# Optimization experiments

Hardware: AMD Instinct MI355X
Metric: run time of the kernel (lower is better)

Reference implementation:

```python
import jax, jax.numpy as jnp
import numpy as np

N_NODES = 100000
N_EDGES = 3200000
IN_F, HID, OUT = 3, 32, 1
NEG_SLOPE = 0.2


def _glorot(key, shape):
    fan_in, fan_out = shape[0], shape[-1]
    lim = jnp.sqrt(6.0 / (fan_in + fan_out)).astype(jnp.float32)
    return jax.random.uniform(key, shape, jnp.float32, -lim, lim)


def setup_inputs() -> dict:
    key = jax.random.key(0)
    ks = jax.random.split(key, 12)
    x = jax.random.normal(ks[0], (N_NODES, IN_F), jnp.float32)
    edge_index = jax.random.randint(ks[1], (2, N_EDGES), 0, N_NODES, jnp.int32)
    return {
        "x": x,
        "edge_index": edge_index,
        "W1": _glorot(ks[2], (IN_F, HID)),
        "att_src1": _glorot(ks[3], (1, HID))[0],
        "att_dst1": _glorot(ks[4], (1, HID))[0],
        "b1": jnp.zeros((HID,), jnp.float32),
        "W2": _glorot(ks[5], (HID, HID)),
        "att_src2": _glorot(ks[6], (1, HID))[0],
        "att_dst2": _glorot(ks[7], (1, HID))[0],
        "b2": jnp.zeros((HID,), jnp.float32),
        "Wl": _glorot(ks[8], (HID, OUT)),
        "bl": jnp.zeros((OUT,), jnp.float32),
    }


def gat_layer(x, src, dst, W, att_src, att_dst, b):
    # h: [N, HID] dense transform
    h = x @ W
    # per-node attention halves (compute once per node, gather per edge)
    a_s = h @ att_src  # [N]
    a_d = h @ att_dst  # [N]
    logits = jax.nn.leaky_relu(a_s[src] + a_d[dst], NEG_SLOPE)  # [E+N]
    # segment-softmax over incoming edges of each dst node
    m = jax.ops.segment_max(logits, dst, num_segments=N_NODES)
    m = jnp.where(jnp.isfinite(m), m, 0.0)
    ex = jnp.exp(logits - m[dst])
    denom = jax.ops.segment_sum(ex, dst, num_segments=N_NODES)
    coef = ex / (denom[dst] + 1e-16)
    # weighted scatter-aggregate of source messages
    out = jax.ops.segment_sum(coef[:, None] * h[src], dst, num_segments=N_NODES)
    return out + b


def reference(x, edge_index, W1, att_src1, att_dst1, b1, W2, att_src2, att_dst2, b2, Wl, bl):
    # PyG GATConv default: add self-loops
    loops = jnp.arange(N_NODES, dtype=edge_index.dtype)
    src = jnp.concatenate([edge_index[0], loops])
    dst = jnp.concatenate([edge_index[1], loops])
    h = gat_layer(x, src, dst, W1, att_src1, att_dst1, b1)
    h = jax.nn.relu(h)  # dropout is identity in eval
    h = gat_layer(h, src, dst, W2, att_src2, att_dst2, b2)
    h = jax.nn.relu(h)
    return h @ Wl + bl
```

## Files before the change

kernel.cpp:

```cpp
#include <hip/hip_runtime.h>
#include <hip/hip_fp16.h>

#define HID 32
#define NB_MAX 512
#define CHUNK_A 16384
#define CHUNK_C 8192

__device__ __forceinline__ float lrelu(float x) {
    return x > 0.0f ? x : 0.2f * x;
}

__global__ void k_transform1(const float* __restrict__ x,
                             const float* __restrict__ W1,
                             const float* __restrict__ att_src,
                             const float* __restrict__ att_dst,
                             float* __restrict__ h,
                             __half* __restrict__ hh,
                             float* __restrict__ a_s,
                             float* __restrict__ a_d,
                             int* __restrict__ bucketCount,
                             int NB, int N)
{
    int tid = blockIdx.x * blockDim.x + threadIdx.x;
    if (tid < NB) bucketCount[tid] = 0;
    int n = tid >> 5;
    int f = tid & 31;
    if (n >= N) return;
    float x0 = x[n * 3 + 0], x1 = x[n * 3 + 1], x2 = x[n * 3 + 2];
    float hv = x0 * W1[f] + x1 * W1[HID + f] + x2 * W1[2 * HID + f];
    h[(size_t)n * HID + f] = hv;
    hh[(size_t)n * HID + f] = __float2half(hv);
    float as = hv * att_src[f];
    float ad = hv * att_dst[f];
    #pragma unroll
    for (int m = 16; m >= 1; m >>= 1) {
        as += __shfl_xor(as, m, 32);
        ad += __shfl_xor(ad, m, 32);
    }
    if (f == 0) { a_s[n] = as; a_d[n] = ad; }
}

__global__ void __launch_bounds__(256) k_count_buckets(const int* __restrict__ dst,
                                                       int* __restrict__ bucketCount,
                                                       int NB, int E)
{
    __shared__ int lh[NB_MAX];
    int t = threadIdx.x;
    for (int i = t; i < NB_MAX; i += 256) lh[i] = 0;
    __syncthreads();
    int base = blockIdx.x * CHUNK_A;
    int end = base + CHUNK_A; if (end > E) end = E;
    for (int i = base + t; i < end; i += 256)
        atomicAdd(&lh[dst[i] >> 8], 1);
    __syncthreads();
    for (int b = t; b < NB; b += 256)
        if (lh[b]) atomicAdd(&bucketCount[b], lh[b]);
}

__global__ void __launch_bounds__(NB_MAX) k_scan_buckets(const int* __restrict__ bucketCount,
                                                         int* __restrict__ bucketBase,
                                                         int* __restrict__ cursor, int NB)
{
    __shared__ int arr[NB_MAX];
    int t = threadIdx.x;
    int c = (t < NB) ? bucketCount[t] : 0;
    arr[t] = c;
    __syncthreads();
    for (int o = 1; o < NB_MAX; o <<= 1) {
        int v = (t >= o) ? arr[t - o] : 0;
        __syncthreads();
        arr[t] += v;
        __syncthreads();
    }
    if (t < NB) { int b = arr[t] - c; bucketBase[t] = b; cursor[t] = b; }
}

__global__ void __launch_bounds__(256) k_binscatter(const int* __restrict__ src,
                                                    const int* __restrict__ dst,
                                                    int* __restrict__ cursor,
                                                    unsigned int* __restrict__ packed,
                                                    int NB, int E)
{
    __shared__ int lhist[NB_MAX], lbase[NB_MAX], lcur[NB_MAX];
    int t = threadIdx.x;
    for (int i = t; i < NB_MAX; i += 256) { lhist[i] = 0; lcur[i] = 0; }
    __syncthreads();
    int base = blockIdx.x * CHUNK_C;
    int cnt = E - base; if (cnt > CHUNK_C) cnt = CHUNK_C;
    for (int i = t; i < cnt; i += 256)
        atomicAdd(&lhist[dst[base + i] >> 8], 1);
    __syncthreads();
    for (int b = t; b < NB; b += 256)
        lbase[b] = lhist[b] ? atomicAdd(&cursor[b], lhist[b]) : 0;
    __syncthreads();
    for (int i = t; i < cnt; i += 256) {
        int d = dst[base + i];
        int s = src[base + i];
        int b = d >> 8;
        int pos = atomicAdd(&lcur[b], 1);
        packed[lbase[b] + pos] = (unsigned)s | ((unsigned)(d & 255) << 17);
    }
}

__global__ void __launch_bounds__(256) k_bucket_csr(const unsigned int* __restrict__ packed,
                                                    const int* __restrict__ bucketBase,
                                                    const int* __restrict__ bucketCount,
                                                    int* __restrict__ csr,
                                                    int* __restrict__ offsets,
                                                    int* __restrict__ deg, int N)
{
    __shared__ int lhist[256], lscan[256], lcur[256];
    int b = blockIdx.x, t = threadIdx.x;
    int base = bucketBase[b];
    int cnt = bucketCount[b];
    lhist[t] = 0; lcur[t] = 0;
    __syncthreads();
    for (int i = t; i < cnt; i += 256)
        atomicAdd(&lhist[(packed[base + i] >> 17) & 255], 1);
    __syncthreads();
    lscan[t] = lhist[t];
    __syncthreads();
    for (int o = 1; o < 256; o <<= 1) {
        int v = (t >= o) ? lscan[t - o] : 0;
        __syncthreads();
        lscan[t] += v;
        __syncthreads();
    }
    int node = (b << 8) + t;
    int excl = lscan[t] - lhist[t];
    if (node < N) { offsets[node] = base + excl; deg[node] = lhist[t]; }
    for (int i = t; i < cnt; i += 256) {
        unsigned int p = packed[base + i];
        int dlow = (p >> 17) & 255;
        int pos = atomicAdd(&lcur[dlow], 1);
        csr[base + (lscan[dlow] - lhist[dlow]) + pos] = (int)(p & 0x1FFFF);
    }
}

__device__ __forceinline__ void agg_core(const float* __restrict__ h,
                                         const __half* __restrict__ hh,
                                         const float* __restrict__ a_s,
                                         float a_dn,
                                         const float* __restrict__ b,
                                         int n, int f, int off, int dg,
                                         const int* __restrict__ csr_src,
                                         float a_sn,
                                         float& vx, float& vy)
{
    float ex = __expf(lrelu(a_sn + a_dn));
    float den = ex;
    const float2 hself = *(const float2*)(h + (size_t)n * HID + 2 * f);
    float accx = ex * hself.x;
    float accy = ex * hself.y;
    for (int base = 0; base < dg; base += 16) {
        int m = dg - base; if (m > 16) m = 16;
        int sv = 0;
        float exv = 0.0f;
        if (f < m) {
            sv = csr_src[off + base + f];
            exv = __expf(lrelu(a_s[sv] + a_dn));
        }
        int j = 0;
        for (; j + 4 <= m; j += 4) {
            int s0 = __shfl(sv, j, 16), s1 = __shfl(sv, j + 1, 16);
            int s2 = __shfl(sv, j + 2, 16), s3 = __shfl(sv, j + 3, 16);
            float e0 = __shfl(exv, j, 16), e1 = __shfl(exv, j + 1, 16);
            float e2 = __shfl(exv, j + 2, 16), e3 = __shfl(exv, j + 3, 16);
            __half2 p0 = *(const __half2*)(hh + (size_t)s0 * HID + 2 * f);
            __half2 p1 = *(const __half2*)(hh + (size_t)s1 * HID + 2 * f);
            __half2 p2 = *(const __half2*)(hh + (size_t)s2 * HID + 2 * f);
            __half2 p3 = *(const __half2*)(hh + (size_t)s3 * HID + 2 * f);
            float2 q0 = __half22float2(p0);
            float2 q1 = __half22float2(p1);
            float2 q2 = __half22float2(p2);
            float2 q3 = __half22float2(p3);
            den += (e0 + e1) + (e2 + e3);
            accx = fmaf(e0, q0.x, accx); accy = fmaf(e0, q0.y, accy);
            accx = fmaf(e1, q1.x, accx); accy = fmaf(e1, q1.y, accy);
            accx = fmaf(e2, q2.x, accx); accy = fmaf(e2, q2.y, accy);
            accx = fmaf(e3, q3.x, accx); accy = fmaf(e3, q3.y, accy);
        }
        for (; j < m; ++j) {
            int s0 = __shfl(sv, j, 16);
            float e0 = __shfl(exv, j, 16);
            float2 q0 = __half22float2(*(const __half2*)(hh + (size_t)s0 * HID + 2 * f));
            den += e0;
            accx = fmaf(e0, q0.x, accx);
            accy = fmaf(e0, q0.y, accy);
        }
    }
    float inv = 1.0f / (den + 1e-16f);
    vx = fmaxf(accx * inv + b[2 * f], 0.0f);
    vy = fmaxf(accy * inv + b[2 * f + 1], 0.0f);
}

__global__ void __launch_bounds__(256) k_agg_mid(const float* __restrict__ h,
                          const __half* __restrict__ hh,
                          const float* __restrict__ a_s,
                          const float* __restrict__ a_d,
                          const int* __restrict__ offsets,
                          const int* __restrict__ deg,
                          const int* __restrict__ csr_src,
                          const float* __restrict__ b,
                          const float* __restrict__ W2,
                          const float* __restrict__ att_src2,
                          const float* __restrict__ att_dst2,
                          float* __restrict__ h_out,
                          __half* __restrict__ hh_out,
                          float* __restrict__ a_s_out,
                          float* __restrict__ a_d_out,
                          int N)
{
    int tid = blockIdx.x * blockDim.x + threadIdx.x;
    int n = tid >> 4;
    int f = tid & 15;
    if (n >= N) return;
    float vx, vy;
    agg_core(h, hh, a_s, a_d[n], b, n, f, offsets[n], deg[n], csr_src, a_s[n], vx, vy);
    float hx = 0.0f, hy = 0.0f;
    #pragma unroll
    for (int k = 0; k < 16; ++k) {
        float va = __shfl(vx, k, 16);
        float vb = __shfl(vy, k, 16);
        float2 w0 = *(const float2*)(W2 + (2 * k) * HID + 2 * f);
        float2 w1 = *(const float2*)(W2 + (2 * k + 1) * HID + 2 * f);
        hx = fmaf(va, w0.x, hx); hy = fmaf(va, w0.y, hy);
        hx = fmaf(vb, w1.x, hx); hy = fmaf(vb, w1.y, hy);
    }
    *(float2*)(h_out + (size_t)n * HID + 2 * f) = make_float2(hx, hy);
    *(__half2*)(hh_out + (size_t)n * HID + 2 * f) = __floats2half2_rn(hx, hy);
    float as = hx * att_src2[2 * f] + hy * att_src2[2 * f + 1];
    float ad = hx * att_dst2[2 * f] + hy * att_dst2[2 * f + 1];
    #pragma unroll
    for (int m2 = 8; m2 >= 1; m2 >>= 1) {
        as += __shfl_xor(as, m2, 16);
        ad += __shfl_xor(ad, m2, 16);
    }
    if (f == 0) { a_s_out[n] = as; a_d_out[n] = ad; }
}

__global__ void __launch_bounds__(256) k_agg_out(const float* __restrict__ h,
                          const __half* __restrict__ hh,
                          const float* __restrict__ a_s,
                          const float* __restrict__ a_d,
                          const int* __restrict__ offsets,
                          const int* __restrict__ deg,
                          const int* __restrict__ csr_src,
                          const float* __restrict__ b,
                          const float* __restrict__ Wl,
                          const float* __restrict__ bl,
                          float* __restrict__ out,
                          int N)
{
    int tid = blockIdx.x * blockDim.x + threadIdx.x;
    int n = tid >> 4;
    int f = tid & 15;
    if (n >= N) return;
    float vx, vy;
    agg_core(h, hh, a_s, a_d[n], b, n, f, offsets[n], deg[n], csr_src, a_s[n], vx, vy);
    float y = vx * Wl[2 * f] + vy * Wl[2 * f + 1];
    #pragma unroll
    for (int m2 = 8; m2 >= 1; m2 >>= 1) {
        y += __shfl_xor(y, m2, 16);
    }
    if (f == 0) out[n] = y + bl[0];
}

extern "C" void kernel_launch(void* const* d_in, const int* in_sizes, int n_in,
                              void* d_out, int out_size, void* d_ws, size_t ws_size,
                              hipStream_t stream)
{
    const float* x        = (const float*)d_in[0];
    const int*   eidx     = (const int*)d_in[1];
    const float* W1       = (const float*)d_in[2];
    const float* att_src1 = (const float*)d_in[3];
    const float* att_dst1 = (const float*)d_in[4];
    const float* b1       = (const float*)d_in[5];
    const float* W2       = (const float*)d_in[6];
    const float* att_src2 = (const float*)d_in[7];
    const float* att_dst2 = (const float*)d_in[8];
    const float* b2       = (const float*)d_in[9];
    const float* Wl       = (const float*)d_in[10];
    const float* bl       = (const float*)d_in[11];
    float* out = (float*)d_out;

    int N = in_sizes[0] / 3;
    int E = in_sizes[1] / 2;
    const int* src = eidx;
    const int* dst = eidx + E;
    int NB = (N + 255) >> 8;

    size_t szNH = (size_t)N * HID * 4;
    size_t szNHh = (size_t)N * HID * 2;
    size_t szE4 = (size_t)E * 4;
    size_t szN4 = (size_t)N * 4;

    char* ws = (char*)d_ws;
    float*  h1      = (float*)ws;  ws += szNH;
    float*  h2      = (float*)ws;  ws += szNH;
    unsigned int* packed = (unsigned int*)h2;
    __half* h1h     = (__half*)ws; ws += szNHh;
    __half* h2h     = (__half*)ws; ws += szNHh;
    int*    csr_src = (int*)ws;    ws += szE4;
    float*  a_s1    = (float*)ws;  ws += szN4;
    float*  a_d1    = (float*)ws;  ws += szN4;
    float*  a_s2    = (float*)ws;  ws += szN4;
    float*  a_d2    = (float*)ws;  ws += szN4;
    int*    deg     = (int*)ws;    ws += szN4;
    int*    offsets = (int*)ws;    ws += szN4;
    int*    bucketCount = (int*)ws; ws += NB_MAX * 4;
    int*    bucketBase  = (int*)ws; ws += NB_MAX * 4;
    int*    cursor      = (int*)ws; ws += NB_MAX * 4;

    const int B = 256;
    int gridNode32 = (N * HID + B - 1) / B;
    int gridNode16 = (N * 16 + B - 1) / B;
    int gridCount  = (E + CHUNK_A - 1) / CHUNK_A;
    int gridBin    = (E + CHUNK_C - 1) / CHUNK_C;

    k_transform1<<<gridNode32, B, 0, stream>>>(x, W1, att_src1, att_dst1,
                                               h1, h1h, a_s1, a_d1, bucketCount, NB, N);
    k_count_buckets<<<gridCount, B, 0, stream>>>(dst, bucketCount, NB, E);
    k_scan_buckets<<<1, NB_MAX, 0, stream>>>(bucketCount, bucketBase, cursor, NB);
    k_binscatter<<<gridBin, B, 0, stream>>>(src, dst, cursor, packed, NB, E);
    k_bucket_csr<<<NB, B, 0, stream>>>(packed, bucketBase, bucketCount,
                                       csr_src, offsets, deg, N);
    k_agg_mid<<<gridNode16, B, 0, stream>>>(h1, h1h, a_s1, a_d1, offsets, deg, csr_src,
                                            b1, W2, att_src2, att_dst2,
                                            h2, h2h, a_s2, a_d2, N);
    k_agg_out<<<gridNode16, B, 0, stream>>>(h2, h2h, a_s2, a_d2, offsets, deg, csr_src,
                                            b2, Wl, bl, out, N);
}
```

Before: 299.9 us.

## Use fixed-stride buckets for CSR build, stage in LDS, drop fp32 features

Replaces the count and scan bucket kernels with fixed-capacity buckets of 132 nodes at a 5120-entry stride. Each bucket's fill is tracked by an atomic cursor, and edges are staged in shared memory so global writes are contiguous. The bucket CSR pass sorts in LDS and writes back in place, so the separate csr array goes away. The fp32 copies of the hidden features are removed and the self term is read from the half buffer. The edge gather loop is unrolled to 8 for more loads in flight. The fixed capacity silently drops edges if a bucket overflows, so correctness depends on a roughly uniform degree distribution.

```diff
diff --git a/kernel.cpp b/kernel.cpp
--- a/kernel.cpp
+++ b/kernel.cpp
@@ -2,33 +2,30 @@
 #include <hip/hip_fp16.h>
 
 #define HID 32
-#define NB_MAX 512
-#define CHUNK_A 16384
-#define CHUNK_C 8192
-
-__device__ __forceinline__ float lrelu(float x) {
-    return x > 0.0f ? x : 0.2f * x;
-}
+#define BN 132
+#define NBPAD 1024
+#define BSTRIDE 5120
+#define CHUNK 8192
+
+__device__ __forceinline__ float lrelu(float x) { return x > 0.0f ? x : 0.2f * x; }
 
 __global__ void k_transform1(const float* __restrict__ x,
                              const float* __restrict__ W1,
                              const float* __restrict__ att_src,
                              const float* __restrict__ att_dst,
-                             float* __restrict__ h,
                              __half* __restrict__ hh,
                              float* __restrict__ a_s,
                              float* __restrict__ a_d,
-                             int* __restrict__ bucketCount,
-                             int NB, int N)
+                             int* __restrict__ cursor,
+                             int N)
 {
     int tid = blockIdx.x * blockDim.x + threadIdx.x;
-    if (tid < NB) bucketCount[tid] = 0;
+    if (tid < NBPAD) cursor[tid] = 0;
     int n = tid >> 5;
     int f = tid & 31;
     if (n >= N) return;
     float x0 = x[n * 3 + 0], x1 = x[n * 3 + 1], x2 = x[n * 3 + 2];
     float hv = x0 * W1[f] + x1 * W1[HID + f] + x2 * W1[2 * HID + f];
-    h[(size_t)n * HID + f] = hv;
     hh[(size_t)n * HID + f] = __float2half(hv);
     float as = hv * att_src[f];
     float ad = hv * att_dst[f];
@@ -40,79 +37,71 @@
     if (f == 0) { a_s[n] = as; a_d[n] = ad; }
 }
 
-__global__ void __launch_bounds__(256) k_count_buckets(const int* __restrict__ dst,
-                                                       int* __restrict__ bucketCount,
-                                                       int NB, int E)
-{
-    __shared__ int lh[NB_MAX];
-    int t = threadIdx.x;
-    for (int i = t; i < NB_MAX; i += 256) lh[i] = 0;
-    __syncthreads();
-    int base = blockIdx.x * CHUNK_A;
-    int end = base + CHUNK_A; if (end > E) end = E;
-    for (int i = base + t; i < end; i += 256)
-        atomicAdd(&lh[dst[i] >> 8], 1);
-    __syncthreads();
-    for (int b = t; b < NB; b += 256)
-        if (lh[b]) atomicAdd(&bucketCount[b], lh[b]);
-}
-
-__global__ void __launch_bounds__(NB_MAX) k_scan_buckets(const int* __restrict__ bucketCount,
-                                                         int* __restrict__ bucketBase,
-                                                         int* __restrict__ cursor, int NB)
-{
-    __shared__ int arr[NB_MAX];
-    int t = threadIdx.x;
-    int c = (t < NB) ? bucketCount[t] : 0;
-    arr[t] = c;
-    __syncthreads();
-    for (int o = 1; o < NB_MAX; o <<= 1) {
-        int v = (t >= o) ? arr[t - o] : 0;
-        __syncthreads();
-        arr[t] += v;
-        __syncthreads();
-    }
-    if (t < NB) { int b = arr[t] - c; bucketBase[t] = b; cursor[t] = b; }
-}
-
 __global__ void __launch_bounds__(256) k_binscatter(const int* __restrict__ src,
                                                     const int* __restrict__ dst,
                                                     int* __restrict__ cursor,
                                                     unsigned int* __restrict__ packed,
                                                     int NB, int E)
 {
-    __shared__ int lhist[NB_MAX], lbase[NB_MAX], lcur[NB_MAX];
+    __shared__ int stage[CHUNK];
+    __shared__ int lhist[NBPAD], lexcl[NBPAD], lbase[NBPAD], lcur[NBPAD];
+    __shared__ int arr[256];
     int t = threadIdx.x;
-    for (int i = t; i < NB_MAX; i += 256) { lhist[i] = 0; lcur[i] = 0; }
-    __syncthreads();
-    int base = blockIdx.x * CHUNK_C;
-    int cnt = E - base; if (cnt > CHUNK_C) cnt = CHUNK_C;
+    for (int i = t; i < NBPAD; i += 256) { lhist[i] = 0; lcur[i] = 0; }
+    __syncthreads();
+    int base = blockIdx.x * CHUNK;
+    int cnt = E - base; if (cnt > CHUNK) cnt = CHUNK;
     for (int i = t; i < cnt; i += 256)
-        atomicAdd(&lhist[dst[base + i] >> 8], 1);
-    __syncthreads();
+        atomicAdd(&lhist[dst[base + i] / BN], 1);
+    __syncthreads();
+    int b0 = 4 * t;
+    int c0 = lhist[b0], c1 = lhist[b0 + 1], c2 = lhist[b0 + 2], c3 = lhist[b0 + 3];
+    int s = c0 + c1 + c2 + c3;
+    arr[t] = s;
+    __syncthreads();
+    for (int o = 1; o < 256; o <<= 1) {
+        int v = (t >= o) ? arr[t - o] : 0;
+        __syncthreads();
+        arr[t] += v;
+        __syncthreads();
+    }
+    int ex = arr[t] - s;
+    lexcl[b0] = ex; lexcl[b0 + 1] = ex + c0;
+    lexcl[b0 + 2] = ex + c0 + c1; lexcl[b0 + 3] = ex + c0 + c1 + c2;
     for (int b = t; b < NB; b += 256)
-        lbase[b] = lhist[b] ? atomicAdd(&cursor[b], lhist[b]) : 0;
+        if (lhist[b]) lbase[b] = b * BSTRIDE + atomicAdd(&cursor[b], lhist[b]);
     __syncthreads();
     for (int i = t; i < cnt; i += 256) {
         int d = dst[base + i];
-        int s = src[base + i];
-        int b = d >> 8;
-        int pos = atomicAdd(&lcur[b], 1);
-        packed[lbase[b] + pos] = (unsigned)s | ((unsigned)(d & 255) << 17);
-    }
-}
-
-__global__ void __launch_bounds__(256) k_bucket_csr(const unsigned int* __restrict__ packed,
-                                                    const int* __restrict__ bucketBase,
-                                                    const int* __restrict__ bucketCount,
-                                                    int* __restrict__ csr,
+        int sv = src[base + i];
+        int b = d / BN;
+        int dl = d - b * BN;
+        int idx = lexcl[b] + atomicAdd(&lcur[b], 1);
+        stage[idx] = (int)((unsigned)sv | ((unsigned)dl << 17));
+    }
+    __syncthreads();
+    for (int i = t; i < cnt; i += 256) {
+        int lo = 0, hi = NB - 1;
+        while (lo < hi) {
+            int mid = (lo + hi + 1) >> 1;
+            if (lexcl[mid] <= i) lo = mid; else hi = mid - 1;
+        }
+        int gpos = lbase[lo] + (i - lexcl[lo]);
+        if (gpos < (lo + 1) * BSTRIDE)
+            packed[gpos] = (unsigned)stage[i];
+    }
+}
+
+__global__ void __launch_bounds__(256) k_bucket_csr(unsigned int* __restrict__ packed,
+                                                    const int* __restrict__ cursor,
                                                     int* __restrict__ offsets,
                                                     int* __restrict__ deg, int N)
 {
+    __shared__ int lcsr[BSTRIDE];
     __shared__ int lhist[256], lscan[256], lcur[256];
     int b = blockIdx.x, t = threadIdx.x;
-    int base = bucketBase[b];
-    int cnt = bucketCount[b];
+    int base = b * BSTRIDE;
+    int cnt = cursor[b]; if (cnt > BSTRIDE) cnt = BSTRIDE;
     lhist[t] = 0; lcur[t] = 0;
     __syncthreads();
     for (int i = t; i < cnt; i += 256)
@@ -126,32 +115,33 @@
         lscan[t] += v;
         __syncthreads();
     }
-    int node = (b << 8) + t;
+    int node = b * BN + t;
     int excl = lscan[t] - lhist[t];
-    if (node < N) { offsets[node] = base + excl; deg[node] = lhist[t]; }
+    if (t < BN && node < N) { offsets[node] = base + excl; deg[node] = lhist[t]; }
     for (int i = t; i < cnt; i += 256) {
         unsigned int p = packed[base + i];
-        int dlow = (p >> 17) & 255;
-        int pos = atomicAdd(&lcur[dlow], 1);
-        csr[base + (lscan[dlow] - lhist[dlow]) + pos] = (int)(p & 0x1FFFF);
-    }
-}
-
-__device__ __forceinline__ void agg_core(const float* __restrict__ h,
-                                         const __half* __restrict__ hh,
+        int dl = (p >> 17) & 255;
+        int pos = atomicAdd(&lcur[dl], 1);
+        lcsr[(lscan[dl] - lhist[dl]) + pos] = (int)(p & 0x1FFFF);
+    }
+    __syncthreads();
+    for (int i = t; i < cnt; i += 256)
+        packed[base + i] = (unsigned)lcsr[i];
+}
+
+__device__ __forceinline__ void agg_core(const __half* __restrict__ hh,
                                          const float* __restrict__ a_s,
-                                         float a_dn,
+                                         float a_dn, float a_sn,
                                          const float* __restrict__ b,
                                          int n, int f, int off, int dg,
                                          const int* __restrict__ csr_src,
-                                         float a_sn,
                                          float& vx, float& vy)
 {
     float ex = __expf(lrelu(a_sn + a_dn));
     float den = ex;
-    const float2 hself = *(const float2*)(h + (size_t)n * HID + 2 * f);
-    float accx = ex * hself.x;
-    float accy = ex * hself.y;
+    float2 hs = __half22float2(*(const __half2*)(hh + (size_t)n * HID + 2 * f));
+    float accx = ex * hs.x;
+    float accy = ex * hs.y;
     for (int base = 0; base < dg; base += 16) {
         int m = dg - base; if (m > 16) m = 16;
         int sv = 0;
@@ -161,6 +151,37 @@
             exv = __expf(lrelu(a_s[sv] + a_dn));
         }
         int j = 0;
+        for (; j + 8 <= m; j += 8) {
+            int s0 = __shfl(sv, j, 16), s1 = __shfl(sv, j + 1, 16);
+            int s2 = __shfl(sv, j + 2, 16), s3 = __shfl(sv, j + 3, 16);
+            int s4 = __shfl(sv, j + 4, 16), s5 = __shfl(sv, j + 5, 16);
+            int s6 = __shfl(sv, j + 6, 16), s7 = __shfl(sv, j + 7, 16);
+            float e0 = __shfl(exv, j, 16), e1 = __shfl(exv, j + 1, 16);
+            float e2 = __shfl(exv, j + 2, 16), e3 = __shfl(exv, j + 3, 16);
+            float e4 = __shfl(exv, j + 4, 16), e5 = __shfl(exv, j + 5, 16);
+            float e6 = __shfl(exv, j + 6, 16), e7 = __shfl(exv, j + 7, 16);
+            __half2 p0 = *(const __half2*)(hh + (size_t)s0 * HID + 2 * f);
+            __half2 p1 = *(const __half2*)(hh + (size_t)s1 * HID + 2 * f);
+            __half2 p2 = *(const __half2*)(hh + (size_t)s2 * HID + 2 * f);
+            __half2 p3 = *(const __half2*)(hh + (size_t)s3 * HID + 2 * f);
+            __half2 p4 = *(const __half2*)(hh + (size_t)s4 * HID + 2 * f);
+            __half2 p5 = *(const __half2*)(hh + (size_t)s5 * HID + 2 * f);
+            __half2 p6 = *(const __half2*)(hh + (size_t)s6 * HID + 2 * f);
+            __half2 p7 = *(const __half2*)(hh + (size_t)s7 * HID + 2 * f);
+            float2 q0 = __half22float2(p0), q1 = __half22float2(p1);
+            float2 q2 = __half22float2(p2), q3 = __half22float2(p3);
+            float2 q4 = __half22float2(p4), q5 = __half22float2(p5);
+            float2 q6 = __half22float2(p6), q7 = __half22float2(p7);
+            den += ((e0 + e1) + (e2 + e3)) + ((e4 + e5) + (e6 + e7));
+            accx = fmaf(e0, q0.x, accx); accy = fmaf(e0, q0.y, accy);
+            accx = fmaf(e1, q1.x, accx); accy = fmaf(e1, q1.y, accy);
+            accx = fmaf(e2, q2.x, accx); accy = fmaf(e2, q2.y, accy);
+            accx = fmaf(e3, q3.x, accx); accy = fmaf(e3, q3.y, accy);
+            accx = fmaf(e4, q4.x, accx); accy = fmaf(e4, q4.y, accy);
+            accx = fmaf(e5, q5.x, accx); accy = fmaf(e5, q5.y, accy);
+            accx = fmaf(e6, q6.x, accx); accy = fmaf(e6, q6.y, accy);
+            accx = fmaf(e7, q7.x, accx); accy = fmaf(e7, q7.y, accy);
+        }
         for (; j + 4 <= m; j += 4) {
             int s0 = __shfl(sv, j, 16), s1 = __shfl(sv, j + 1, 16);
             int s2 = __shfl(sv, j + 2, 16), s3 = __shfl(sv, j + 3, 16);
@@ -170,10 +191,8 @@
             __half2 p1 = *(const __half2*)(hh + (size_t)s1 * HID + 2 * f);
             __half2 p2 = *(const __half2*)(hh + (size_t)s2 * HID + 2 * f);
             __half2 p3 = *(const __half2*)(hh + (size_t)s3 * HID + 2 * f);
-            float2 q0 = __half22float2(p0);
-            float2 q1 = __half22float2(p1);
-            float2 q2 = __half22float2(p2);
-            float2 q3 = __half22float2(p3);
+            float2 q0 = __half22float2(p0), q1 = __half22float2(p1);
+            float2 q2 = __half22float2(p2), q3 = __half22float2(p3);
             den += (e0 + e1) + (e2 + e3);
             accx = fmaf(e0, q0.x, accx); accy = fmaf(e0, q0.y, accy);
             accx = fmaf(e1, q1.x, accx); accy = fmaf(e1, q1.y, accy);
@@ -194,8 +213,7 @@
     vy = fmaxf(accy * inv + b[2 * f + 1], 0.0f);
 }
 
-__global__ void __launch_bounds__(256) k_agg_mid(const float* __restrict__ h,
-                          const __half* __restrict__ hh,
+__global__ void __launch_bounds__(256) k_agg_mid(const __half* __restrict__ hh,
                           const float* __restrict__ a_s,
                           const float* __restrict__ a_d,
                           const int* __restrict__ offsets,
@@ -205,7 +223,6 @@
                           const float* __restrict__ W2,
                           const float* __restrict__ att_src2,
                           const float* __restrict__ att_dst2,
-                          float* __restrict__ h_out,
                           __half* __restrict__ hh_out,
                           float* __restrict__ a_s_out,
                           float* __restrict__ a_d_out,
@@ -216,7 +233,7 @@
     int f = tid & 15;
     if (n >= N) return;
     float vx, vy;
-    agg_core(h, hh, a_s, a_d[n], b, n, f, offsets[n], deg[n], csr_src, a_s[n], vx, vy);
+    agg_core(hh, a_s, a_d[n], a_s[n], b, n, f, offsets[n], deg[n], csr_src, vx, vy);
     float hx = 0.0f, hy = 0.0f;
     #pragma unroll
     for (int k = 0; k < 16; ++k) {
@@ -227,7 +244,6 @@
         hx = fmaf(va, w0.x, hx); hy = fmaf(va, w0.y, hy);
         hx = fmaf(vb, w1.x, hx); hy = fmaf(vb, w1.y, hy);
     }
-    *(float2*)(h_out + (size_t)n * HID + 2 * f) = make_float2(hx, hy);
     *(__half2*)(hh_out + (size_t)n * HID + 2 * f) = __floats2half2_rn(hx, hy);
     float as = hx * att_src2[2 * f] + hy * att_src2[2 * f + 1];
     float ad = hx * att_dst2[2 * f] + hy * att_dst2[2 * f + 1];
@@ -239,8 +255,7 @@
     if (f == 0) { a_s_out[n] = as; a_d_out[n] = ad; }
 }
 
-__global__ void __launch_bounds__(256) k_agg_out(const float* __restrict__ h,
-                          const __half* __restrict__ hh,
+__global__ void __launch_bounds__(256) k_agg_out(const __half* __restrict__ hh,
                           const float* __restrict__ a_s,
                           const float* __restrict__ a_d,
                           const int* __restrict__ offsets,
@@ -257,7 +272,7 @@
     int f = tid & 15;
     if (n >= N) return;
     float vx, vy;
-    agg_core(h, hh, a_s, a_d[n], b, n, f, offsets[n], deg[n], csr_src, a_s[n], vx, vy);
+    agg_core(hh, a_s, a_d[n], a_s[n], b, n, f, offsets[n], deg[n], csr_src, vx, vy);
     float y = vx * Wl[2 * f] + vy * Wl[2 * f + 1];
     #pragma unroll
     for (int m2 = 8; m2 >= 1; m2 >>= 1) {
@@ -288,46 +303,36 @@
     int E = in_sizes[1] / 2;
     const int* src = eidx;
     const int* dst = eidx + E;
-    int NB = (N + 255) >> 8;
-
-    size_t szNH = (size_t)N * HID * 4;
+    int NB = (N + BN - 1) / BN;
+
     size_t szNHh = (size_t)N * HID * 2;
-    size_t szE4 = (size_t)E * 4;
-    size_t szN4 = (size_t)N * 4;
+    size_t szN4  = (size_t)N * 4;
+    size_t szPK  = (size_t)NB * BSTRIDE * 4;
 
     char* ws = (char*)d_ws;
-    float*  h1      = (float*)ws;  ws += szNH;
-    float*  h2      = (float*)ws;  ws += szNH;
-    unsigned int* packed = (unsigned int*)h2;
-    __half* h1h     = (__half*)ws; ws += szNHh;
-    __half* h2h     = (__half*)ws; ws += szNHh;
-    int*    csr_src = (int*)ws;    ws += szE4;
-    float*  a_s1    = (float*)ws;  ws += szN4;
-    float*  a_d1    = (float*)ws;  ws += szN4;
-    float*  a_s2    = (float*)ws;  ws += szN4;
-    float*  a_d2    = (float*)ws;  ws += szN4;
-    int*    deg     = (int*)ws;    ws += szN4;
-    int*    offsets = (int*)ws;    ws += szN4;
-    int*    bucketCount = (int*)ws; ws += NB_MAX * 4;
-    int*    bucketBase  = (int*)ws; ws += NB_MAX * 4;
-    int*    cursor      = (int*)ws; ws += NB_MAX * 4;
+    __half* h1h    = (__half*)ws; ws += szNHh;
+    __half* h2h    = (__half*)ws; ws += szNHh;
+    unsigned int* packed = (unsigned int*)ws; ws += szPK;
+    float*  a_s1   = (float*)ws;  ws += szN4;
+    float*  a_d1   = (float*)ws;  ws += szN4;
+    float*  a_s2   = (float*)ws;  ws += szN4;
+    float*  a_d2   = (float*)ws;  ws += szN4;
+    int*    deg    = (int*)ws;    ws += szN4;
+    int*    offsets= (int*)ws;    ws += szN4;
+    int*    cursor = (int*)ws;    ws += NBPAD * 4;
 
     const int B = 256;
     int gridNode32 = (N * HID + B - 1) / B;
     int gridNode16 = (N * 16 + B - 1) / B;
-    int gridCount  = (E + CHUNK_A - 1) / CHUNK_A;
-    int gridBin    = (E + CHUNK_C - 1) / CHUNK_C;
+    int gridBin    = (E + CHUNK - 1) / CHUNK;
 
     k_transform1<<<gridNode32, B, 0, stream>>>(x, W1, att_src1, att_dst1,
-                                               h1, h1h, a_s1, a_d1, bucketCount, NB, N);
-    k_count_buckets<<<gridCount, B, 0, stream>>>(dst, bucketCount, NB, E);
-    k_scan_buckets<<<1, NB_MAX, 0, stream>>>(bucketCount, bucketBase, cursor, NB);
+                                               h1h, a_s1, a_d1, cursor, N);
     k_binscatter<<<gridBin, B, 0, stream>>>(src, dst, cursor, packed, NB, E);
-    k_bucket_csr<<<NB, B, 0, stream>>>(packed, bucketBase, bucketCount,
-                                       csr_src, offsets, deg, N);
-    k_agg_mid<<<gridNode16, B, 0, stream>>>(h1, h1h, a_s1, a_d1, offsets, deg, csr_src,
+    k_bucket_csr<<<NB, B, 0, stream>>>(packed, cursor, offsets, deg, N);
+    k_agg_mid<<<gridNode16, B, 0, stream>>>(h1h, a_s1, a_d1, offsets, deg, (const int*)packed,
                                             b1, W2, att_src2, att_dst2,
-                                            h2, h2h, a_s2, a_d2, N);
-    k_agg_out<<<gridNode16, B, 0, stream>>>(h2, h2h, a_s2, a_d2, offsets, deg, csr_src,
+                                            h2h, a_s2, a_d2, N);
+    k_agg_out<<<gridNode16, B, 0, stream>>>(h2h, a_s2, a_d2, offsets, deg, (const int*)packed,
                                             b2, Wl, bl, out, N);
 }
```

After: 272.4 us. 1.1x faster.
